# Kernel optimization log

Hardware: AMD Instinct MI355X
Metric: run time of the kernel (lower is better)

The kernel has to match this reference:

```python
import jax, jax.numpy as jnp
import numpy as np

NX, NY, C = 784, 480, 32
N0 = NX * NY          # 376320 level-0 nodes
N1 = N0 // 4          # 94080
N2 = N0 // 16         # 23520


def _gcn(x, w, b, ei, n):
    """PyG GCNConv: add self loops, symmetric norm, linear, scatter-sum, bias."""
    loop = jnp.arange(n, dtype=ei.dtype)
    src = jnp.concatenate([ei[0], loop])
    dst = jnp.concatenate([ei[1], loop])
    deg = jax.ops.segment_sum(jnp.ones(src.shape[0], x.dtype), dst, num_segments=n)
    dinv = jnp.where(deg > 0, jax.lax.rsqrt(deg), 0.0)
    norm = (dinv[src] * dinv[dst])[:, None]          # [E+n, 1]
    msg = (x @ w)[src] * norm                        # gather + scale
    return jax.ops.segment_sum(msg, dst, num_segments=n) + b


def _up2(x, h, w):
    """2x nearest-neighbor upsample of a row-major-flattened (h, w, C) grid."""
    g = x.reshape(h, w, x.shape[-1])
    return jnp.repeat(jnp.repeat(g, 2, axis=0), 2, axis=1).reshape(-1, x.shape[-1])


def setup_inputs() -> dict:
    key = jax.random.key(0)
    ks = jax.random.split(key, 20)
    f32 = jnp.float32
    inp = {
        "x": jax.random.normal(ks[0], (N0, 4), f32),
        "fc1_w": jax.random.normal(ks[1], (4, C), f32) * 0.1,
        "fc1_b": jax.random.normal(ks[2], (C,), f32) * 0.1,
        "w1": jax.random.normal(ks[3], (C, C), f32) * 0.1,
        "b1": jax.random.normal(ks[4], (C,), f32) * 0.1,
        "w2": jax.random.normal(ks[5], (C, C), f32) * 0.1,
        "b2": jax.random.normal(ks[6], (C,), f32) * 0.1,
        "w3": jax.random.normal(ks[7], (C, C), f32) * 0.1,
        "b3": jax.random.normal(ks[8], (C,), f32) * 0.1,
        "w4": jax.random.normal(ks[9], (C, C), f32) * 0.1,
        "b4": jax.random.normal(ks[10], (C,), f32) * 0.1,
        "w5": jax.random.normal(ks[11], (C, C), f32) * 0.1,
        "b5": jax.random.normal(ks[12], (C,), f32) * 0.1,
        "fc2_w": jax.random.normal(ks[13], (C, 3), f32) * 0.1,
        "fc2_b": jax.random.normal(ks[14], (3,), f32) * 0.1,
        "idx0": jnp.arange(N0, dtype=jnp.int32),
        "idx1": jnp.arange(N1, dtype=jnp.int32),
        "idx2": jnp.arange(N2, dtype=jnp.int32),
        "ei0": jax.random.randint(ks[15], (2, 4 * N0), 0, N0, dtype=jnp.int32),
        "ei1": jax.random.randint(ks[16], (2, 4 * N1), 0, N1, dtype=jnp.int32),
        "ei2": jax.random.randint(ks[17], (2, 4 * N2), 0, N2, dtype=jnp.int32),
    }
    return inp


def reference(x, fc1_w, fc1_b, w1, b1, w2, b2, w3, b3, w4, b4, w5, b5,
              fc2_w, fc2_b, idx0, idx1, idx2, ei0, ei1, ei2):
    h = jax.nn.relu(x @ fc1_w + fc1_b)                                  # [N0, 32]
    h = h.at[idx0].set(_gcn(h[idx0], w1, b1, ei0, idx0.shape[0]))
    h = jax.nn.relu(h)
    # level-1 downsample: take every other grid row/col
    h1 = h.reshape(NX, NY, C)[::2, ::2].reshape(-1, C)                  # [N1, 32]
    h1 = h1.at[idx1].set(_gcn(h1[idx1], w2, b2, ei1, idx1.shape[0]))
    h1 = jax.nn.relu(h1)
    # level-2 downsample
    h2 = h1.reshape(NX // 2, NY // 2, C)[::2, ::2].reshape(-1, C)       # [N2, 32]
    h2 = h2.at[idx2].set(_gcn(h2[idx2], w3, b3, ei2, idx2.shape[0]))
    h2 = jax.nn.relu(h2)
    # upsample level-2 -> level-1, residual add
    h1u = h1 + _up2(h2, NX // 4, NY // 4)
    h1u = h1u.at[idx1].set(_gcn(h1u[idx1], w4, b4, ei1, idx1.shape[0]))
    h1u = jax.nn.relu(h1u)
    # upsample level-1 -> level-0, residual add
    hu = h + _up2(h1u, NX // 2, NY // 2)
    hu = hu.at[idx0].set(_gcn(hu[idx0], w5, b5, ei0, idx0.shape[0]))
    hu = jax.nn.relu(hu)
    return (hu @ fc2_w + fc2_b)[idx0]                                   # [N0, 3]
```

## Files before the change

kernel.cpp:

```cpp
#include <hip/hip_runtime.h>
#include <hip/hip_bf16.h>

typedef unsigned short u16;
typedef unsigned int u32;
typedef float fx2 __attribute__((ext_vector_type(2)));

#define NXg 784
#define NYg 480
constexpr int N0c = NXg * NYg;
constexpr int N1c = N0c / 4;
constexpr int N2c = N0c / 16;
constexpr int NTc = N0c + N1c + N2c;
constexpr int E0c = 4 * N0c;
constexpr int E1c = 4 * N1c;
constexpr int E2c = 4 * N2c;
constexpr int Etot = E0c + E1c + E2c;
constexpr int P0c = E0c + 3 * N0c;
constexpr int P1c = E1c + 3 * N1c;
constexpr int P2c = E2c + 3 * N2c;
constexpr int Ptot = P0c + P1c + P2c;
constexpr int NB0 = (N0c + 1023) / 1024;
constexpr int NB1 = (N1c + 1023) / 1024;
constexpr int NB2 = (N2c + 1023) / 1024;
constexpr int NBt = NB0 + NB1 + NB2;

__device__ __forceinline__ float bf2f(u16 v) {
    union { u32 u; float f; } t; t.u = ((u32)v) << 16; return t.f;
}
__device__ __forceinline__ u16 f2bf(float f) {
    union { float f; u32 u; } t; t.f = f;
    u32 u = t.u;
    u32 r = (u + 0x7fffu + ((u >> 16) & 1u)) >> 16;
    return (u16)r;
}
__device__ __forceinline__ float rdf(const void* p, int i, int isf32) {
    if (isf32) return ((const float*)p)[i];
    return bf2f(((const u16*)p)[i]);
}
__device__ __forceinline__ void stage(float* dst, const void* src, int n, int isf32) {
    int t = threadIdx.x;
    if (isf32) {
        const float* s = (const float*)src;
        for (int i = t; i < n; i += 256) dst[i] = s[i];
    } else {
        const u16* s = (const u16*)src;
        for (int i = t; i < n; i += 256) dst[i] = bf2f(s[i]);
    }
}

struct F32S {
    typedef float T;
    static __device__ __forceinline__ float ld(const T* p, size_t i) { return p[i]; }
    static __device__ __forceinline__ void st(T* p, size_t i, float v) { p[i] = v; }
    static __device__ __forceinline__ fx2 ld2(const T* p, size_t i) {
        return ((const fx2*)p)[i];
    }
};
struct BF16S {
    typedef u16 T;
    static __device__ __forceinline__ float ld(const T* p, size_t i) { return bf2f(p[i]); }
    static __device__ __forceinline__ void st(T* p, size_t i, float v) { p[i] = f2bf(v); }
    static __device__ __forceinline__ fx2 ld2(const T* p, size_t i) {
        u32 w = ((const u32*)p)[i];
        fx2 r; r.x = bf2f((u16)(w & 0xffffu)); r.y = bf2f((u16)(w >> 16));
        return r;
    }
};

__device__ __forceinline__ void lvl_of_bin(int b, int& lv, int& bl) {
    if (b < NB0) { lv = 0; bl = b; }
    else if (b < NB0 + NB1) { lv = 1; bl = b - NB0; }
    else { lv = 2; bl = b - NB0 - NB1; }
}

__global__ void k_detect(const u32* __restrict__ xw, int* __restrict__ flag) {
    __shared__ int cnt;
    if (threadIdx.x == 0) cnt = 0;
    __syncthreads();
    u32 w = xw[threadIdx.x];
    int e = (int)((w >> 7) & 0xFFu);
    int hit = ((e >= 90 && e <= 135) || ((w & 0x7FFFu) == 0u)) ? 1 : 0;
    atomicAdd(&cnt, hit);
    __syncthreads();
    if (threadIdx.x == 0) *flag = (cnt < 192) ? 1 : 0;
}

__global__ void k_init(int* __restrict__ binCnt, u16* __restrict__ y0,
                       u16* __restrict__ y1, u16* __restrict__ y2) {
    int t = blockIdx.x * blockDim.x + threadIdx.x;
    if (t < NBt) binCnt[t] = 0;
    if (t < 32) { y0[t] = 0; y1[t] = 0; y2[t] = 0; }
}

__global__ void kA_count(const int* __restrict__ ei0, const int* __restrict__ ei1,
                         const int* __restrict__ ei2, int* __restrict__ binCnt) {
    __shared__ int lc[NB0];
    int b = blockIdx.x, t = threadIdx.x;
    int lv, bl; lvl_of_bin(b, lv, bl);
    const int* dstp; int E, nb, binB;
    if (lv == 0) { dstp = ei0 + E0c; E = E0c; nb = NB0; binB = 0; }
    else if (lv == 1) { dstp = ei1 + E1c; E = E1c; nb = NB1; binB = NB0; }
    else { dstp = ei2 + E2c; E = E2c; nb = NB2; binB = NB0 + NB1; }
    for (int i = t; i < nb; i += 256) lc[i] = 0;
    __syncthreads();
    int e0 = bl * 4096, e1 = min(E, e0 + 4096);
    for (int i = e0 + t; i < e1; i += 256) atomicAdd(&lc[dstp[i] >> 10], 1);
    __syncthreads();
    for (int i = t; i < nb; i += 256) if (lc[i]) atomicAdd(&binCnt[binB + i], lc[i]);
}

__global__ void kB_scan(const int* __restrict__ binCnt, int* __restrict__ binStart,
                        int* __restrict__ binCursor) {
    __shared__ int s[512];
    int t = threadIdx.x;
    int v = (t < NBt) ? binCnt[t] : 0;
    s[t] = v;
    __syncthreads();
    for (int off = 1; off < 512; off <<= 1) {
        int x = (t >= off) ? s[t - off] : 0;
        __syncthreads();
        s[t] += x;
        __syncthreads();
    }
    if (t < NBt) { int e = s[t] - v; binStart[t] = e; binCursor[t] = e; }
    if (t == 0) binStart[NBt] = Etot;
}

__global__ void kC_place(const int* __restrict__ ei0, const int* __restrict__ ei1,
                         const int* __restrict__ ei2, int* __restrict__ binCursor,
                         int2* __restrict__ BE) {
    __shared__ int lc[NB0];
    __shared__ int lb[NB0];
    int b = blockIdx.x, t = threadIdx.x;
    int lv, bl; lvl_of_bin(b, lv, bl);
    const int* srcp; const int* dstp; int E, nb, binB;
    if (lv == 0) { srcp = ei0; dstp = ei0 + E0c; E = E0c; nb = NB0; binB = 0; }
    else if (lv == 1) { srcp = ei1; dstp = ei1 + E1c; E = E1c; nb = NB1; binB = NB0; }
    else { srcp = ei2; dstp = ei2 + E2c; E = E2c; nb = NB2; binB = NB0 + NB1; }
    for (int i = t; i < nb; i += 256) lc[i] = 0;
    __syncthreads();
    int e0 = bl * 4096, e1 = min(E, e0 + 4096);
    for (int i = e0 + t; i < e1; i += 256) atomicAdd(&lc[dstp[i] >> 10], 1);
    __syncthreads();
    for (int i = t; i < nb; i += 256) {
        int c = lc[i];
        lb[i] = c ? atomicAdd(&binCursor[binB + i], c) : 0;
        lc[i] = 0;
    }
    __syncthreads();
    for (int i = e0 + t; i < e1; i += 256) {
        int d = dstp[i];
        int bn = d >> 10;
        int p = atomicAdd(&lc[bn], 1);
        BE[lb[bn] + p] = make_int2(srcp[i], d);
    }
}

__global__ void kD1_count(const int2* __restrict__ BE, const int* __restrict__ binStart,
                          int* __restrict__ CNT, float* __restrict__ DINV,
                          int* __restrict__ binPadTot) {
    __shared__ int lc[1024];
    __shared__ int red[256];
    int b = blockIdx.x, t = threadIdx.x;
    int lv, bl; lvl_of_bin(b, lv, bl);
    int cbase, nLev;
    if (lv == 0) { cbase = 0; nLev = N0c; }
    else if (lv == 1) { cbase = N0c; nLev = N1c; }
    else { cbase = N0c + N1c; nLev = N2c; }
    for (int i = t; i < 1024; i += 256) lc[i] = 0;
    __syncthreads();
    int s0 = binStart[b], s1 = binStart[b + 1];
    for (int i = s0 + t; i < s1; i += 256) {
        int2 e = BE[i];
        atomicAdd(&lc[e.y & 1023], 1);
    }
    __syncthreads();
    int nodeB = bl << 10;
    int ps = 0;
#pragma unroll
    for (int j = 0; j < 4; j++) {
        int li = t * 4 + j;
        int node = nodeB + li;
        if (node < nLev) {
            int c = lc[li];
            CNT[cbase + node] = c;
            DINV[cbase + node] = rsqrtf((float)c + 1.0f);
            ps += (c + 3) & ~3;
        }
    }
    red[t] = ps;
    __syncthreads();
    for (int off = 128; off > 0; off >>= 1) {
        if (t < off) red[t] += red[t + off];
        __syncthreads();
    }
    if (t == 0) binPadTot[b] = red[0];
}

__global__ void kD2_scan(const int* __restrict__ binPadTot, int* __restrict__ binPadStart) {
    __shared__ int s[512];
    __shared__ int tot0, tot01;
    int t = threadIdx.x;
    int v = (t < NBt) ? binPadTot[t] : 0;
    s[t] = v;
    __syncthreads();
    for (int off = 1; off < 512; off <<= 1) {
        int x = (t >= off) ? s[t - off] : 0;
        __syncthreads();
        s[t] += x;
        __syncthreads();
    }
    if (t == 0) { tot0 = s[NB0 - 1]; tot01 = s[NB0 + NB1 - 1]; }
    __syncthreads();
    if (t < NBt) {
        int ex = s[t] - v;
        int cb, sub;
        if (t < NB0) { cb = 0; sub = 0; }
        else if (t < NB0 + NB1) { cb = P0c; sub = tot0; }
        else { cb = P0c + P1c; sub = tot01; }
        binPadStart[t] = cb + ex - sub;
    }
}

__global__ void kD3_final(const int2* __restrict__ BE, const int* __restrict__ binStart,
                          const int* __restrict__ CNT, const int* __restrict__ binPadStart,
                          int* __restrict__ rowptr, int* __restrict__ colAll) {
    __shared__ int lst[1024];
    __shared__ int lcur[1024];
    __shared__ int red[256];
    int b = blockIdx.x, t = threadIdx.x;
    int lv, bl; lvl_of_bin(b, lv, bl);
    int cbase, nLev, dummy;
    if (lv == 0) { cbase = 0; nLev = N0c; dummy = N0c; }
    else if (lv == 1) { cbase = N0c; nLev = N1c; dummy = N1c; }
    else { cbase = N0c + N1c; nLev = N2c; dummy = N2c; }
    int nodeB = bl << 10;
    int pc[4];
    int ps = 0;
#pragma unroll
    for (int j = 0; j < 4; j++) {
        int li = t * 4 + j;
        int node = nodeB + li;
        int c = (node < nLev) ? CNT[cbase + node] : 0;
        pc[j] = (c + 3) & ~3;
        ps += pc[j];
    }
    red[t] = ps;
    __syncthreads();
    for (int off = 1; off < 256; off <<= 1) {
        int x = (t >= off) ? red[t - off] : 0;
        __syncthreads();
        red[t] += x;
        __syncthreads();
    }
    int ex = red[t] - ps;
    int tot = red[255];
    int off = ex;
#pragma unroll
    for (int j = 0; j < 4; j++) {
        int li = t * 4 + j;
        lst[li] = off;
        lcur[li] = off;
        off += pc[j];
    }
    int cb = binPadStart[b];
#pragma unroll
    for (int j = 0; j < 4; j++) {
        int li = t * 4 + j;
        int node = nodeB + li;
        if (node < nLev) rowptr[cbase + node] = cb + lst[li];
    }
    __syncthreads();
    for (int i = t; i < tot; i += 256) colAll[cb + i] = dummy;
    __syncthreads();
    int s0 = binStart[b], s1 = binStart[b + 1];
    for (int i = s0 + t; i < s1; i += 256) {
        int2 e = BE[i];
        int p = atomicAdd(&lcur[e.y & 1023], 1);
        colAll[cb + p] = e.x;
    }
}

template <class SIn>
__device__ __forceinline__ fx2 gather2(const typename SIn::T* __restrict__ ys,
                                       const int* __restrict__ rp,
                                       const int* __restrict__ cnt,
                                       const int* __restrict__ col,
                                       const float* __restrict__ dinv,
                                       int node, int cp) {
    int s0 = rp[node];
    int nch = (cnt[node] + 3) >> 2;
    fx2 a = SIn::ld2(ys, (size_t)node * 16 + cp);
    const int4* c4 = (const int4*)(col + s0);
    for (int i = 0; i < nch; i++) {
        int4 cs = c4[i];
        fx2 a0 = SIn::ld2(ys, (size_t)cs.x * 16 + cp);
        fx2 a1 = SIn::ld2(ys, (size_t)cs.y * 16 + cp);
        fx2 a2 = SIn::ld2(ys, (size_t)cs.z * 16 + cp);
        fx2 a3 = SIn::ld2(ys, (size_t)cs.w * 16 + cp);
        a += (a0 + a1) + (a2 + a3);
    }
    float di = dinv[node];
    a *= di;
    return a;
}

constexpr int FC1_TILES = N0c / 64;
__global__ void k_fc1prep(const void* __restrict__ x, const void* __restrict__ fw,
                          const void* __restrict__ fb, const void* __restrict__ w1,
                          const float* __restrict__ d0, u16* __restrict__ ys1,
                          const int* __restrict__ flag) {
    int isf32 = *flag;
    __shared__ float sx[256];
    __shared__ float sh[64 * 33];
    __shared__ float sfw[128];
    __shared__ float sfb[32];
    __shared__ float sw1[1024];
    int t = threadIdx.x;
    stage(sw1, w1, 1024, isf32);
    stage(sfw, fw, 128, isf32);
    stage(sfb, fb, 32, isf32);
    __syncthreads();
    int c = t & 31;
    int ng = t >> 5;
    int ci0 = t & 15;
    int rgrp = t >> 4;
    for (int tile = blockIdx.x; tile < FC1_TILES; tile += gridDim.x) {
        int nodeBase = tile * 64;
        sx[t] = rdf(x, nodeBase * 4 + t, isf32);
        __syncthreads();
#pragma unroll
        for (int i = 0; i < 8; i++) {
            int ln = ng + i * 8;
            float a = sfb[c];
#pragma unroll
            for (int k = 0; k < 4; k++) a = fmaf(sx[ln * 4 + k], sfw[k * 32 + c], a);
            sh[ln * 33 + c] = fmaxf(a, 0.0f);
        }
        __syncthreads();
        float acc[4][2];
#pragma unroll
        for (int r = 0; r < 4; r++) { acc[r][0] = 0.0f; acc[r][1] = 0.0f; }
#pragma unroll
        for (int k = 0; k < 32; k++) {
            float w0 = sw1[k * 32 + ci0];
            float w1v = sw1[k * 32 + ci0 + 16];
#pragma unroll
            for (int r = 0; r < 4; r++) {
                float s = sh[(rgrp * 4 + r) * 33 + k];
                acc[r][0] = fmaf(s, w0, acc[r][0]);
                acc[r][1] = fmaf(s, w1v, acc[r][1]);
            }
        }
#pragma unroll
        for (int r = 0; r < 4; r++) {
            int node = nodeBase + rgrp * 4 + r;
            float dv = d0[node];
            BF16S::st(ys1, (size_t)node * 32 + ci0, acc[r][0] * dv);
            BF16S::st(ys1, (size_t)node * 32 + ci0 + 16, acc[r][1] * dv);
        }
        __syncthreads();
    }
}

template <class SIn, class SOut, int NPB>
__global__ void k_gds(const typename SIn::T* __restrict__ ys_in, const int* __restrict__ rp,
                      const int* __restrict__ cnt, const int* __restrict__ col,
                      const float* __restrict__ dinv_p, const void* __restrict__ b,
                      float* __restrict__ O, const void* __restrict__ wn,
                      const float* __restrict__ dinv_c, typename SOut::T* __restrict__ ys_out,
                      int cols, const int* __restrict__ flag) {
    int isf32 = *flag;
    __shared__ float sv[NPB * 32];
    __shared__ float swn[1024];
    int t = threadIdx.x;
    int nodeBase = blockIdx.x * NPB;
    int rb = nodeBase / cols;
    if (!(rb & 1)) stage(swn, wn, 1024, isf32);
    int cp = t & 15;
#pragma unroll
    for (int i = 0; i < NPB / 16; i++) {
        int local = (t >> 4) + i * 16;
        int node = nodeBase + local;
        fx2 g = gather2<SIn>(ys_in, rp, cnt, col, dinv_p, node, cp);
        fx2 v;
        v.x = fmaxf(g.x + rdf(b, 2 * cp, isf32), 0.0f);
        v.y = fmaxf(g.y + rdf(b, 2 * cp + 1, isf32), 0.0f);
        __builtin_nontemporal_store(v, (fx2*)O + (size_t)node * 16 + cp);
        sv[local * 32 + 2 * cp] = v.x;
        sv[local * 32 + 2 * cp + 1] = v.y;
    }
    __syncthreads();
    if (!(rb & 1)) {
#pragma unroll
        for (int i = 0; i < NPB / 16; i++) {
            int item = t + i * 256;
            int childIdx = item >> 5;
            int ci = item & 31;
            int lc = childIdx * 2;
            int cc = (nodeBase - rb * cols) + lc;
            int dn = (rb >> 1) * (cols >> 1) + (cc >> 1);
            float a = 0.0f;
#pragma unroll
            for (int k = 0; k < 32; k++) a = fmaf(sv[lc * 32 + k], swn[k * 32 + ci], a);
            SOut::st(ys_out, (size_t)dn * 32 + ci, a * dinv_c[dn]);
        }
    }
}

template <class SIn, class SOut, int NPB>
__global__ void k_gup(const typename SIn::T* __restrict__ ys_in, const int* __restrict__ rp,
                      const int* __restrict__ cnt, const int* __restrict__ col,
                      const float* __restrict__ dinv_p, const void* __restrict__ b,
                      const float* __restrict__ R, const void* __restrict__ wn,
                      const float* __restrict__ dinv_c, typename SOut::T* __restrict__ ys_out,
                      int cols_p, const int* __restrict__ flag) {
    constexpr int RPT = NPB / 4;
    int isf32 = *flag;
    __shared__ float sv[NPB * 32];
    __shared__ float sch[NPB * 4 * 33];
    __shared__ float swn[1024];
    int t = threadIdx.x;
    int nodeBase = blockIdx.x * NPB;
    stage(swn, wn, 1024, isf32);
    if (t < NPB * 16) {
        int local = t >> 4, cp = t & 15;
        int node = nodeBase + local;
        fx2 g = gather2<SIn>(ys_in, rp, cnt, col, dinv_p, node, cp);
        sv[local * 32 + 2 * cp] = fmaxf(g.x + rdf(b, 2 * cp, isf32), 0.0f);
        sv[local * 32 + 2 * cp + 1] = fmaxf(g.y + rdf(b, 2 * cp + 1, isf32), 0.0f);
    }
    __syncthreads();
    int rb = nodeBase / cols_p;
    int ccb = nodeBase - rb * cols_p;
    int cols_c = cols_p * 2;
#pragma unroll
    for (int i = 0; i < NPB / 2; i++) {
        int item = t + i * 256;
        int row = item >> 5, k = item & 31;
        int lp = row >> 2, j = row & 3;
        int ch = (2 * rb + (j >> 1)) * cols_c + 2 * (ccb + lp) + (j & 1);
        sch[row * 33 + k] = R[(size_t)ch * 32 + k] + sv[lp * 32 + k];
    }
    __syncthreads();
    int ci0 = t & 15;
    int rgrp = t >> 4;
    float acc[RPT][2];
#pragma unroll
    for (int r = 0; r < RPT; r++) { acc[r][0] = 0.0f; acc[r][1] = 0.0f; }
#pragma unroll
    for (int k = 0; k < 32; k++) {
        float w0 = swn[k * 32 + ci0];
        float w1v = swn[k * 32 + ci0 + 16];
#pragma unroll
        for (int r = 0; r < RPT; r++) {
            float s = sch[(rgrp * RPT + r) * 33 + k];
            acc[r][0] = fmaf(s, w0, acc[r][0]);
            acc[r][1] = fmaf(s, w1v, acc[r][1]);
        }
    }
#pragma unroll
    for (int r = 0; r < RPT; r++) {
        int row = rgrp * RPT + r;
        int lp = row >> 2, j = row & 3;
        int ch = (2 * rb + (j >> 1)) * cols_c + 2 * (ccb + lp) + (j & 1);
        float dc = dinv_c[ch];
        SOut::st(ys_out, (size_t)ch * 32 + ci0, acc[r][0] * dc);
        SOut::st(ys_out, (size_t)ch * 32 + ci0 + 16, acc[r][1] * dc);
    }
}

__global__ void k_gfc2(const u16* __restrict__ ys, const int* __restrict__ rp,
                       const int* __restrict__ cnt, const int* __restrict__ col,
                       const float* __restrict__ dinv, const void* __restrict__ b5,
                       const void* __restrict__ fw, const void* __restrict__ fb,
                       void* __restrict__ out, int n, const int* __restrict__ flag) {
    int isf32 = *flag;
    __shared__ float sv[1024];
    __shared__ float sw[96];
    __shared__ float sfb[3];
    int t = threadIdx.x;
    if (t < 96) sw[t] = rdf(fw, t, isf32);
    if (t < 3) sfb[t] = rdf(fb, t, isf32);
    int nodeBase = blockIdx.x * 32;
    int cp = t & 15;
#pragma unroll
    for (int i = 0; i < 2; i++) {
        int local = (t >> 4) + i * 16;
        int node = nodeBase + local;
        fx2 g = gather2<BF16S>(ys, rp, cnt, col, dinv, node, cp);
        sv[local * 32 + 2 * cp] = fmaxf(g.x + rdf(b5, 2 * cp, isf32), 0.0f);
        sv[local * 32 + 2 * cp + 1] = fmaxf(g.y + rdf(b5, 2 * cp + 1, isf32), 0.0f);
    }
    __syncthreads();
    if (t < 96) {
        int ln = t / 3, j = t - ln * 3;
        int gn = nodeBase + ln;
        float o = sfb[j];
#pragma unroll
        for (int k = 0; k < 32; k++) o = fmaf(sv[ln * 32 + k], sw[k * 3 + j], o);
        if (isf32) ((float*)out)[(size_t)gn * 3 + j] = o;
        else ((u16*)out)[(size_t)gn * 3 + j] = f2bf(o);
    }
}

extern "C" void kernel_launch(void* const* d_in, const int* in_sizes, int n_in,
                              void* d_out, int out_size, void* d_ws, size_t ws_size,
                              hipStream_t stream) {
    const void* x    = d_in[0];
    const void* fc1w = d_in[1];
    const void* fc1b = d_in[2];
    const void* w1 = d_in[3];  const void* b1 = d_in[4];
    const void* w2 = d_in[5];  const void* b2 = d_in[6];
    const void* w3 = d_in[7];  const void* b3 = d_in[8];
    const void* w4 = d_in[9];  const void* b4 = d_in[10];
    const void* w5 = d_in[11]; const void* b5 = d_in[12];
    const void* fc2w = d_in[13]; const void* fc2b = d_in[14];
    const int* ei0 = (const int*)d_in[18];
    const int* ei1 = (const int*)d_in[19];
    const int* ei2 = (const int*)d_in[20];

    u16* YS0 = (u16*)d_ws;
    float* A   = (float*)(YS0 + (size_t)(N0c + 1) * 32);
    u16* YS1   = (u16*)(A + (size_t)N0c * 32);
    float* H1  = (float*)(YS1 + (size_t)(N1c + 1) * 32);
    u16* YS2   = (u16*)(H1 + (size_t)N1c * 32);
    float* DINV = (float*)(YS2 + (size_t)(N2c + 1) * 32);
    int* CNT   = (int*)(DINV + NTc);
    int* RPA   = CNT + NTc;
    int* COLA  = RPA + NTc;
    int2* BE   = (int2*)(COLA + Ptot);
    int* binCnt      = (int*)(BE + Etot);
    int* binStart    = binCnt + NBt;
    int* binCursor   = binStart + NBt + 1;
    int* binPadTot   = binCursor + NBt;
    int* binPadStart = binPadTot + NBt;
    int* FLAG        = binPadStart + NBt;

    float* D0 = DINV; float* D1 = D0 + N0c; float* D2 = D1 + N1c;
    int* C0 = CNT;  int* C1 = C0 + N0c;  int* C2 = C1 + N1c;
    int* RP0 = RPA; int* RP1 = RP0 + N0c; int* RP2 = RP1 + N1c;

    const int Bk = 256;

    k_detect<<<1, 256, 0, stream>>>((const u32*)x, FLAG);
    k_init<<<2, 256, 0, stream>>>(binCnt, YS0 + (size_t)N0c * 32,
                                  YS1 + (size_t)N1c * 32, YS2 + (size_t)N2c * 32);

    kA_count<<<NBt, Bk, 0, stream>>>(ei0, ei1, ei2, binCnt);
    kB_scan<<<1, 512, 0, stream>>>(binCnt, binStart, binCursor);
    kC_place<<<NBt, Bk, 0, stream>>>(ei0, ei1, ei2, binCursor, BE);
    kD1_count<<<NBt, Bk, 0, stream>>>(BE, binStart, CNT, DINV, binPadTot);
    kD2_scan<<<1, 512, 0, stream>>>(binPadTot, binPadStart);
    kD3_final<<<NBt, Bk, 0, stream>>>(BE, binStart, CNT, binPadStart, RPA, COLA);

    k_fc1prep<<<1960, Bk, 0, stream>>>(x, fc1w, fc1b, w1, D0, YS0, FLAG);
    k_gds<BF16S, BF16S, 32><<<N0c / 32, Bk, 0, stream>>>(YS0, RP0, C0, COLA, D0, b1, A, w2, D1, YS1, NYg, FLAG);
    k_gds<BF16S, BF16S, 16><<<N1c / 16, Bk, 0, stream>>>(YS1, RP1, C1, COLA, D1, b2, H1, w3, D2, YS2, NYg / 2, FLAG);
    k_gup<BF16S, BF16S, 8><<<N2c / 8, Bk, 0, stream>>>(YS2, RP2, C2, COLA, D2, b3, H1, w4, D1, YS1, NYg / 4, FLAG);
    k_gup<BF16S, BF16S, 16><<<N1c / 16, Bk, 0, stream>>>(YS1, RP1, C1, COLA, D1, b4, A, w5, D0, YS0, NYg / 2, FLAG);
    k_gfc2<<<N0c / 32, Bk, 0, stream>>>(YS0, RP0, C0, COLA, D0, b5, fc2w, fc2b, d_out, N0c, FLAG);
}
```

Baseline: 356.1 us.

## Store residual activations in bf16, pack edge records, merge init kernels

```diff
diff --git a/kernel.cpp b/kernel.cpp
--- a/kernel.cpp
+++ b/kernel.cpp
@@ -55,6 +55,9 @@
     static __device__ __forceinline__ fx2 ld2(const T* p, size_t i) {
         return ((const fx2*)p)[i];
     }
+    static __device__ __forceinline__ void st2nt(T* p, size_t i, fx2 v) {
+        __builtin_nontemporal_store(v, (fx2*)p + i);
+    }
 };
 struct BF16S {
     typedef u16 T;
@@ -65,6 +68,10 @@
         fx2 r; r.x = bf2f((u16)(w & 0xffffu)); r.y = bf2f((u16)(w >> 16));
         return r;
     }
+    static __device__ __forceinline__ void st2nt(T* p, size_t i, fx2 v) {
+        u32 w = (u32)f2bf(v.x) | ((u32)f2bf(v.y) << 16);
+        __builtin_nontemporal_store(w, (u32*)p + i);
+    }
 };
 
 __device__ __forceinline__ void lvl_of_bin(int b, int& lv, int& bl) {
@@ -73,23 +80,24 @@
     else { lv = 2; bl = b - NB0 - NB1; }
 }
 
-__global__ void k_detect(const u32* __restrict__ xw, int* __restrict__ flag) {
+__global__ void k_dinit(const u32* __restrict__ xw, int* __restrict__ flag,
+                        int* __restrict__ binCnt, u16* __restrict__ y0,
+                        u16* __restrict__ y1, u16* __restrict__ y2) {
     __shared__ int cnt;
-    if (threadIdx.x == 0) cnt = 0;
-    __syncthreads();
-    u32 w = xw[threadIdx.x];
-    int e = (int)((w >> 7) & 0xFFu);
-    int hit = ((e >= 90 && e <= 135) || ((w & 0x7FFFu) == 0u)) ? 1 : 0;
-    atomicAdd(&cnt, hit);
-    __syncthreads();
-    if (threadIdx.x == 0) *flag = (cnt < 192) ? 1 : 0;
-}
-
-__global__ void k_init(int* __restrict__ binCnt, u16* __restrict__ y0,
-                       u16* __restrict__ y1, u16* __restrict__ y2) {
-    int t = blockIdx.x * blockDim.x + threadIdx.x;
-    if (t < NBt) binCnt[t] = 0;
-    if (t < 32) { y0[t] = 0; y1[t] = 0; y2[t] = 0; }
+    int t = threadIdx.x;
+    int g = blockIdx.x * 256 + t;
+    if (blockIdx.x == 0) {
+        if (t == 0) cnt = 0;
+        __syncthreads();
+        u32 w = xw[t];
+        int e = (int)((w >> 7) & 0xFFu);
+        int hit = ((e >= 90 && e <= 135) || ((w & 0x7FFFu) == 0u)) ? 1 : 0;
+        atomicAdd(&cnt, hit);
+        __syncthreads();
+        if (t == 0) *flag = (cnt < 192) ? 1 : 0;
+    }
+    if (g < NBt) binCnt[g] = 0;
+    if (blockIdx.x == 1 && t < 32) { y0[t] = 0; y1[t] = 0; y2[t] = 0; }
 }
 
 __global__ void kA_count(const int* __restrict__ ei0, const int* __restrict__ ei1,
@@ -128,7 +136,7 @@
 
 __global__ void kC_place(const int* __restrict__ ei0, const int* __restrict__ ei1,
                          const int* __restrict__ ei2, int* __restrict__ binCursor,
-                         int2* __restrict__ BE) {
+                         u32* __restrict__ BE) {
     __shared__ int lc[NB0];
     __shared__ int lb[NB0];
     int b = blockIdx.x, t = threadIdx.x;
@@ -152,11 +160,11 @@
         int d = dstp[i];
         int bn = d >> 10;
         int p = atomicAdd(&lc[bn], 1);
-        BE[lb[bn] + p] = make_int2(srcp[i], d);
-    }
-}
-
-__global__ void kD1_count(const int2* __restrict__ BE, const int* __restrict__ binStart,
+        BE[lb[bn] + p] = ((u32)srcp[i] << 10) | (u32)(d & 1023);
+    }
+}
+
+__global__ void kD1_count(const u32* __restrict__ BE, const int* __restrict__ binStart,
                           int* __restrict__ CNT, float* __restrict__ DINV,
                           int* __restrict__ binPadTot) {
     __shared__ int lc[1024];
@@ -171,8 +179,7 @@
     __syncthreads();
     int s0 = binStart[b], s1 = binStart[b + 1];
     for (int i = s0 + t; i < s1; i += 256) {
-        int2 e = BE[i];
-        atomicAdd(&lc[e.y & 1023], 1);
+        atomicAdd(&lc[BE[i] & 1023u], 1);
     }
     __syncthreads();
     int nodeB = bl << 10;
@@ -222,7 +229,7 @@
     }
 }
 
-__global__ void kD3_final(const int2* __restrict__ BE, const int* __restrict__ binStart,
+__global__ void kD3_final(const u32* __restrict__ BE, const int* __restrict__ binStart,
                           const int* __restrict__ CNT, const int* __restrict__ binPadStart,
                           int* __restrict__ rowptr, int* __restrict__ colAll) {
     __shared__ int lst[1024];
@@ -275,9 +282,9 @@
     __syncthreads();
     int s0 = binStart[b], s1 = binStart[b + 1];
     for (int i = s0 + t; i < s1; i += 256) {
-        int2 e = BE[i];
-        int p = atomicAdd(&lcur[e.y & 1023], 1);
-        colAll[cb + p] = e.x;
+        u32 e = BE[i];
+        int p = atomicAdd(&lcur[e & 1023u], 1);
+        colAll[cb + p] = (int)(e >> 10);
     }
 }
 
@@ -363,11 +370,11 @@
     }
 }
 
-template <class SIn, class SOut, int NPB>
+template <class SIn, class SRes, class SOut, int NPB>
 __global__ void k_gds(const typename SIn::T* __restrict__ ys_in, const int* __restrict__ rp,
                       const int* __restrict__ cnt, const int* __restrict__ col,
                       const float* __restrict__ dinv_p, const void* __restrict__ b,
-                      float* __restrict__ O, const void* __restrict__ wn,
+                      typename SRes::T* __restrict__ O, const void* __restrict__ wn,
                       const float* __restrict__ dinv_c, typename SOut::T* __restrict__ ys_out,
                       int cols, const int* __restrict__ flag) {
     int isf32 = *flag;
@@ -386,7 +393,7 @@
         fx2 v;
         v.x = fmaxf(g.x + rdf(b, 2 * cp, isf32), 0.0f);
         v.y = fmaxf(g.y + rdf(b, 2 * cp + 1, isf32), 0.0f);
-        __builtin_nontemporal_store(v, (fx2*)O + (size_t)node * 16 + cp);
+        SRes::st2nt(O, (size_t)node * 16 + cp, v);
         sv[local * 32 + 2 * cp] = v.x;
         sv[local * 32 + 2 * cp + 1] = v.y;
     }
@@ -408,11 +415,11 @@
     }
 }
 
-template <class SIn, class SOut, int NPB>
+template <class SIn, class SRes, class SOut, int NPB>
 __global__ void k_gup(const typename SIn::T* __restrict__ ys_in, const int* __restrict__ rp,
                       const int* __restrict__ cnt, const int* __restrict__ col,
                       const float* __restrict__ dinv_p, const void* __restrict__ b,
-                      const float* __restrict__ R, const void* __restrict__ wn,
+                      const typename SRes::T* __restrict__ R, const void* __restrict__ wn,
                       const float* __restrict__ dinv_c, typename SOut::T* __restrict__ ys_out,
                       int cols_p, const int* __restrict__ flag) {
     constexpr int RPT = NPB / 4;
@@ -440,7 +447,7 @@
         int row = item >> 5, k = item & 31;
         int lp = row >> 2, j = row & 3;
         int ch = (2 * rb + (j >> 1)) * cols_c + 2 * (ccb + lp) + (j & 1);
-        sch[row * 33 + k] = R[(size_t)ch * 32 + k] + sv[lp * 32 + k];
+        sch[row * 33 + k] = SRes::ld(R, (size_t)ch * 32 + k) + sv[lp * 32 + k];
     }
     __syncthreads();
     int ci0 = t & 15;
@@ -521,15 +528,15 @@
     const int* ei2 = (const int*)d_in[20];
 
     u16* YS0 = (u16*)d_ws;
-    float* A   = (float*)(YS0 + (size_t)(N0c + 1) * 32);
-    u16* YS1   = (u16*)(A + (size_t)N0c * 32);
-    float* H1  = (float*)(YS1 + (size_t)(N1c + 1) * 32);
-    u16* YS2   = (u16*)(H1 + (size_t)N1c * 32);
+    u16* A   = YS0 + (size_t)(N0c + 1) * 32;
+    u16* YS1 = A + (size_t)N0c * 32;
+    u16* H1  = YS1 + (size_t)(N1c + 1) * 32;
+    u16* YS2 = H1 + (size_t)N1c * 32;
     float* DINV = (float*)(YS2 + (size_t)(N2c + 1) * 32);
     int* CNT   = (int*)(DINV + NTc);
     int* RPA   = CNT + NTc;
     int* COLA  = RPA + NTc;
-    int2* BE   = (int2*)(COLA + Ptot);
+    u32* BE    = (u32*)(COLA + Ptot);
     int* binCnt      = (int*)(BE + Etot);
     int* binStart    = binCnt + NBt;
     int* binCursor   = binStart + NBt + 1;
@@ -543,9 +550,9 @@
 
     const int Bk = 256;
 
-    k_detect<<<1, 256, 0, stream>>>((const u32*)x, FLAG);
-    k_init<<<2, 256, 0, stream>>>(binCnt, YS0 + (size_t)N0c * 32,
-                                  YS1 + (size_t)N1c * 32, YS2 + (size_t)N2c * 32);
+    k_dinit<<<2, Bk, 0, stream>>>((const u32*)x, FLAG, binCnt,
+                                  YS0 + (size_t)N0c * 32, YS1 + (size_t)N1c * 32,
+                                  YS2 + (size_t)N2c * 32);
 
     kA_count<<<NBt, Bk, 0, stream>>>(ei0, ei1, ei2, binCnt);
     kB_scan<<<1, 512, 0, stream>>>(binCnt, binStart, binCursor);
@@ -555,9 +562,9 @@
     kD3_final<<<NBt, Bk, 0, stream>>>(BE, binStart, CNT, binPadStart, RPA, COLA);
 
     k_fc1prep<<<1960, Bk, 0, stream>>>(x, fc1w, fc1b, w1, D0, YS0, FLAG);
-    k_gds<BF16S, BF16S, 32><<<N0c / 32, Bk, 0, stream>>>(YS0, RP0, C0, COLA, D0, b1, A, w2, D1, YS1, NYg, FLAG);
-    k_gds<BF16S, BF16S, 16><<<N1c / 16, Bk, 0, stream>>>(YS1, RP1, C1, COLA, D1, b2, H1, w3, D2, YS2, NYg / 2, FLAG);
-    k_gup<BF16S, BF16S, 8><<<N2c / 8, Bk, 0, stream>>>(YS2, RP2, C2, COLA, D2, b3, H1, w4, D1, YS1, NYg / 4, FLAG);
-    k_gup<BF16S, BF16S, 16><<<N1c / 16, Bk, 0, stream>>>(YS1, RP1, C1, COLA, D1, b4, A, w5, D0, YS0, NYg / 2, FLAG);
+    k_gds<BF16S, BF16S, BF16S, 32><<<N0c / 32, Bk, 0, stream>>>(YS0, RP0, C0, COLA, D0, b1, A, w2, D1, YS1, NYg, FLAG);
+    k_gds<BF16S, BF16S, BF16S, 16><<<N1c / 16, Bk, 0, stream>>>(YS1, RP1, C1, COLA, D1, b2, H1, w3, D2, YS2, NYg / 2, FLAG);
+    k_gup<BF16S, BF16S, BF16S, 8><<<N2c / 8, Bk, 0, stream>>>(YS2, RP2, C2, COLA, D2, b3, H1, w4, D1, YS1, NYg / 4, FLAG);
+    k_gup<BF16S, BF16S, BF16S, 16><<<N1c / 16, Bk, 0, stream>>>(YS1, RP1, C1, COLA, D1, b4, A, w5, D0, YS0, NYg / 2, FLAG);
     k_gfc2<<<N0c / 32, Bk, 0, stream>>>(YS0, RP0, C0, COLA, D0, b5, fc2w, fc2b, d_out, N0c, FLAG);
 }
```

Result: no change. 351.4 us (-1.3%).
